# Optimization experiments

Hardware: AMD Instinct MI355X
Metric: run time of the kernel (lower is better)

## Reference

```python
import jax, jax.numpy as jnp
import numpy as np

NUM_HEADS = 8
CHUNK = 64
TOP_K = 5


def setup_inputs() -> dict:
    key = jax.random.key(0)
    ks = jax.random.split(key, 5)
    D = 512
    x = jax.random.normal(ks[0], (1, 2048, D), dtype=jnp.float32)
    s = 0.02
    Wq = jax.random.normal(ks[1], (D, D), dtype=jnp.float32) * s
    Wk = jax.random.normal(ks[2], (D, D), dtype=jnp.float32) * s
    Wv = jax.random.normal(ks[3], (D, D), dtype=jnp.float32) * s
    Wo = jax.random.normal(ks[4], (D, D), dtype=jnp.float32) * s
    return {"x": x, "Wq": Wq, "Wk": Wk, "Wv": Wv, "Wo": Wo}


def reference(x, Wq, Wk, Wv, Wo):
    B, S, D = x.shape
    H = NUM_HEADS
    hd = D // H
    scale = hd ** -0.5
    C = S // CHUNK  # number of chunks

    def split_heads(t):
        return t.reshape(B, S, H, hd).transpose(0, 2, 1, 3)  # [B,H,S,hd]

    Q = split_heads(x @ Wq)
    K = split_heads(x @ Wk)
    V = split_heads(x @ Wv)

    # chunked K/V: [B,H,C,chunk,hd]
    Kc = K.reshape(B, H, C, CHUNK, hd)
    Vc = V.reshape(B, H, C, CHUNK, hd)

    # chunk descriptors: mean-pooled keys per chunk -> [B,H,C,hd]
    chunk_keys = Kc.mean(axis=3)

    # route each query to top-k chunks by scaled similarity
    sims = jnp.einsum('bhsd,bhcd->bhsc', Q, chunk_keys) * scale  # [B,H,S,C]
    _, idx = jax.lax.top_k(sims, TOP_K)  # [B,H,S,K]

    # gather selected K/V chunk blocks: [B,H,S,K,chunk,hd]
    idx_flat = idx.reshape(B, H, S * TOP_K)[:, :, :, None, None]
    Kg = jnp.take_along_axis(Kc, idx_flat, axis=2).reshape(B, H, S, TOP_K, CHUNK, hd)
    Vg = jnp.take_along_axis(Vc, idx_flat, axis=2).reshape(B, H, S, TOP_K, CHUNK, hd)

    # sparse block attention over the K*chunk gathered keys per query
    scores = jnp.einsum('bhsd,bhskcd->bhskc', Q, Kg) * scale
    attn = jax.nn.softmax(scores.reshape(B, H, S, TOP_K * CHUNK), axis=-1)
    attn = attn.reshape(B, H, S, TOP_K, CHUNK)
    out = jnp.einsum('bhskc,bhskcd->bhsd', attn, Vg)  # [B,H,S,hd]

    out = out.transpose(0, 2, 1, 3).reshape(B, S, D)
    return out @ Wo
```

## Files before the change

### kernel.cpp

```cpp
#include <hip/hip_runtime.h>
#include <hip/hip_bf16.h>
#include <math.h>

#define S_LEN 2048
#define D_DIM 512
#define H_NUM 8
#define HD    64
#define C_NUM 32
#define TOPK  5
#define SCALE 0.125f
#define QCAP  1024
#define ATILES 16

typedef __attribute__((ext_vector_type(8))) short bf16x8;
typedef __attribute__((ext_vector_type(4))) float f32x4;
typedef __attribute__((ext_vector_type(4))) unsigned short us4;

__device__ __forceinline__ unsigned short f2b(float f) {
    __hip_bfloat16 h = __float2bfloat16(f);
    unsigned short u;
    __builtin_memcpy(&u, &h, 2);
    return u;
}
__device__ __forceinline__ bf16x8 pack8(float4 a, float4 b) {
    bf16x8 r;
    r[0] = (short)f2b(a.x); r[1] = (short)f2b(a.y);
    r[2] = (short)f2b(a.z); r[3] = (short)f2b(a.w);
    r[4] = (short)f2b(b.x); r[5] = (short)f2b(b.y);
    r[6] = (short)f2b(b.z); r[7] = (short)f2b(b.w);
    return r;
}
__device__ __forceinline__ float b2f(unsigned short u) {
    __hip_bfloat16 h;
    __builtin_memcpy(&h, &u, 2);
    return __bfloat162float(h);
}

#define BM 64
#define BN 64
#define BK 32

__device__ __forceinline__ void gemm_body(const float* __restrict__ A,
                                          const float* __restrict__ B,
                                          float* __restrict__ C,
                                          int M, int N, int K,
                                          int bx, int by) {
    __shared__ float As[BK][BM + 4];
    __shared__ float Bs[BK][BN];

    const int t  = threadIdx.x;
    const int tx = t & 15;
    const int ty = t >> 4;
    const int m0 = by * BM;
    const int n0 = bx * BN;

    float4 acc0 = make_float4(0.f,0.f,0.f,0.f);
    float4 acc1 = make_float4(0.f,0.f,0.f,0.f);
    float4 acc2 = make_float4(0.f,0.f,0.f,0.f);
    float4 acc3 = make_float4(0.f,0.f,0.f,0.f);

    const int ar = t >> 3;
    const int ac = (t & 7) * 4;
    const int br = t >> 4;
    const int bc = (t & 15) * 4;

    float4 a0, a1, b0, b1;
    auto LD = [&](int k0) {
        a0 = *(const float4*)&A[(size_t)(m0 + ar)      * K + k0 + ac];
        a1 = *(const float4*)&A[(size_t)(m0 + ar + 32) * K + k0 + ac];
        b0 = *(const float4*)&B[(size_t)(k0 + br)      * N + n0 + bc];
        b1 = *(const float4*)&B[(size_t)(k0 + br + 16) * N + n0 + bc];
    };

    LD(0);
    for (int k0 = 0; k0 < K; k0 += BK) {
        __syncthreads();
        As[ac+0][ar]    = a0.x; As[ac+1][ar]    = a0.y; As[ac+2][ar]    = a0.z; As[ac+3][ar]    = a0.w;
        As[ac+0][ar+32] = a1.x; As[ac+1][ar+32] = a1.y; As[ac+2][ar+32] = a1.z; As[ac+3][ar+32] = a1.w;
        *(float4*)&Bs[br][bc]      = b0;
        *(float4*)&Bs[br + 16][bc] = b1;
        __syncthreads();

        if (k0 + BK < K) LD(k0 + BK);

        #pragma unroll
        for (int kk = 0; kk < BK; ++kk) {
            float4 a = *(const float4*)&As[kk][ty * 4];
            float4 b = *(const float4*)&Bs[kk][tx * 4];
            acc0.x += a.x*b.x; acc0.y += a.x*b.y; acc0.z += a.x*b.z; acc0.w += a.x*b.w;
            acc1.x += a.y*b.x; acc1.y += a.y*b.y; acc1.z += a.y*b.z; acc1.w += a.y*b.w;
            acc2.x += a.z*b.x; acc2.y += a.z*b.y; acc2.z += a.z*b.z; acc2.w += a.z*b.w;
            acc3.x += a.w*b.x; acc3.y += a.w*b.y; acc3.z += a.w*b.z; acc3.w += a.w*b.w;
        }
    }

    *(float4*)&C[(size_t)(m0 + ty*4 + 0) * N + n0 + tx*4] = acc0;
    *(float4*)&C[(size_t)(m0 + ty*4 + 1) * N + n0 + tx*4] = acc1;
    *(float4*)&C[(size_t)(m0 + ty*4 + 2) * N + n0 + tx*4] = acc2;
    *(float4*)&C[(size_t)(m0 + ty*4 + 3) * N + n0 + tx*4] = acc3;
}

__global__ __launch_bounds__(256) void gemm_qkv(const float* __restrict__ A,
                                                const float* __restrict__ Wq,
                                                const float* __restrict__ Wk,
                                                float* __restrict__ Qb,
                                                float* __restrict__ Kb) {
    const float* B = (blockIdx.z == 0) ? Wq : Wk;
    float*       C = (blockIdx.z == 0) ? Qb : Kb;
    gemm_body(A, B, C, S_LEN, D_DIM, D_DIM, blockIdx.x, blockIdx.y);
}

template <bool ABF16, bool CBF16>
__device__ __forceinline__ void gemm_bf16_body(const void* __restrict__ Aptr,
                                               const float* __restrict__ B,
                                               void* __restrict__ Cptr,
                                               int M, int N, int K,
                                               int bx, int by) {
    __shared__ unsigned short As[64][72];
    __shared__ unsigned short Bs[64][72];

    const int t  = threadIdx.x;
    const int m0 = by * 64;
    const int n0 = bx * 64;
    const int rl = t >> 2;
    const int c4 = (t & 3) * 16;

    const int lane = t & 63, w = t >> 6, lr = lane & 15, quad = lane >> 4;

    f32x4 acc[4] = {{0.f,0.f,0.f,0.f},{0.f,0.f,0.f,0.f},
                    {0.f,0.f,0.f,0.f},{0.f,0.f,0.f,0.f}};

    float4 fa[4]; bf16x8 ba[2]; float4 fb[4];
    auto LDA = [&](int k0) {
        if (ABF16) {
            const unsigned short* A = (const unsigned short*)Aptr;
            ba[0] = *(const bf16x8*)&A[(size_t)(m0 + rl) * K + k0 + c4];
            ba[1] = *(const bf16x8*)&A[(size_t)(m0 + rl) * K + k0 + c4 + 8];
        } else {
            const float* A = (const float*)Aptr;
            const float* p = &A[(size_t)(m0 + rl) * K + k0 + c4];
            fa[0] = *(const float4*)&p[0];  fa[1] = *(const float4*)&p[4];
            fa[2] = *(const float4*)&p[8];  fa[3] = *(const float4*)&p[12];
        }
    };
    auto LDB = [&](int k0) {
        const float* p = &B[(size_t)(k0 + rl) * N + n0 + c4];
        fb[0] = *(const float4*)&p[0];  fb[1] = *(const float4*)&p[4];
        fb[2] = *(const float4*)&p[8];  fb[3] = *(const float4*)&p[12];
    };

    LDA(0); LDB(0);
    for (int k0 = 0; k0 < K; k0 += 64) {
        __syncthreads();
        if (ABF16) {
            *(bf16x8*)&As[rl][c4]     = ba[0];
            *(bf16x8*)&As[rl][c4 + 8] = ba[1];
        } else {
            *(bf16x8*)&As[rl][c4]     = pack8(fa[0], fa[1]);
            *(bf16x8*)&As[rl][c4 + 8] = pack8(fa[2], fa[3]);
        }
        #pragma unroll
        for (int f = 0; f < 4; ++f) {
            float4 v = fb[f];
            Bs[c4 + f*4 + 0][rl] = f2b(v.x);
            Bs[c4 + f*4 + 1][rl] = f2b(v.y);
            Bs[c4 + f*4 + 2][rl] = f2b(v.z);
            Bs[c4 + f*4 + 3][rl] = f2b(v.w);
        }
        __syncthreads();

        if (k0 + 64 < K) { LDA(k0 + 64); LDB(k0 + 64); }

        bf16x8 a0 = *(const bf16x8*)&As[w * 16 + lr][quad * 8];
        bf16x8 a1 = *(const bf16x8*)&As[w * 16 + lr][32 + quad * 8];
        #pragma unroll
        for (int nt = 0; nt < 4; ++nt) {
            bf16x8 b0 = *(const bf16x8*)&Bs[nt * 16 + lr][quad * 8];
            bf16x8 b1 = *(const bf16x8*)&Bs[nt * 16 + lr][32 + quad * 8];
            acc[nt] = __builtin_amdgcn_mfma_f32_16x16x32_bf16(a0, b0, acc[nt], 0, 0, 0);
            acc[nt] = __builtin_amdgcn_mfma_f32_16x16x32_bf16(a1, b1, acc[nt], 0, 0, 0);
        }
    }

    #pragma unroll
    for (int nt = 0; nt < 4; ++nt)
        #pragma unroll
        for (int r = 0; r < 4; ++r) {
            int m = m0 + w * 16 + quad * 4 + r;
            int n = n0 + nt * 16 + lr;
            if (CBF16) ((unsigned short*)Cptr)[(size_t)m * N + n] = f2b(acc[nt][r]);
            else       ((float*)Cptr)[(size_t)m * N + n] = acc[nt][r];
        }
}

__global__ __launch_bounds__(256) void gemm_v(const float* __restrict__ x,
                                              const float* __restrict__ Wv,
                                              unsigned short* __restrict__ Vbf,
                                              int* __restrict__ cur) {
    if (blockIdx.x == 0 && blockIdx.y == 0) cur[threadIdx.x] = 0;
    gemm_bf16_body<false, true>(x, Wv, Vbf, S_LEN, D_DIM, D_DIM,
                                blockIdx.x, blockIdx.y);
}

__global__ __launch_bounds__(256) void gemm_out(const unsigned short* __restrict__ Obn,
                                                const float* __restrict__ Wo,
                                                float* __restrict__ out) {
    gemm_bf16_body<true, false>(Obn, Wo, out, S_LEN, D_DIM, D_DIM,
                                blockIdx.x, blockIdx.y);
}

__global__ __launch_bounds__(256) void chunk_keys_kernel(const float* __restrict__ K,
                                                         float* __restrict__ ck) {
    int i = blockIdx.x * 256 + threadIdx.x;
    int c = i >> 9;
    int d = i & 511;
    const float* p = K + (size_t)c * 64 * D_DIM + d;
    float sum = 0.f;
    #pragma unroll
    for (int r = 0; r < 64; ++r) sum += p[(size_t)r * D_DIM];
    ck[(size_t)c * D_DIM + d] = sum * (1.0f / 64.0f);
}

__global__ __launch_bounds__(256) void sims_topk(const float* __restrict__ Q,
                                                 const float* __restrict__ ck,
                                                 int* __restrict__ cur,
                                                 unsigned short* __restrict__ qlist) {
    __shared__ float qtile[64][68];
    __shared__ float cks[32][68];
    __shared__ float simsb[64][36];
    __shared__ int   lds_cnt[32];
    __shared__ int   lds_base[32];

    const int t  = threadIdx.x;
    const int s0 = blockIdx.x * 64;
    const int h  = blockIdx.y;

    if (t < 32) lds_cnt[t] = 0;

    {
        int r = t >> 2;
        #pragma unroll
        for (int i = 0; i < 4; ++i) {
            int cf4 = (t & 3) * 4 + i;
            *(float4*)&qtile[r][cf4 * 4] =
                *(const float4*)&Q[(size_t)(s0 + r) * D_DIM + h * HD + cf4 * 4];
        }
    }
    for (int i = t; i < C_NUM * 16; i += 256) {
        int c = i >> 4, df4 = i & 15;
        *(float4*)&cks[c][df4 * 4] =
            *(const float4*)&ck[(size_t)c * D_DIM + h * HD + df4 * 4];
    }
    __syncthreads();

    {
        const int sl = t >> 2, g = t & 3;
        float sa[8] = {0.f,0.f,0.f,0.f,0.f,0.f,0.f,0.f};
        #pragma unroll
        for (int d4 = 0; d4 < 16; ++d4) {
            float4 q4 = *(const float4*)&qtile[sl][d4 * 4];
            #pragma unroll
            for (int j = 0; j < 8; ++j) {
                float4 c4 = *(const float4*)&cks[g * 8 + j][d4 * 4];
                sa[j] += q4.x*c4.x + q4.y*c4.y + q4.z*c4.z + q4.w*c4.w;
            }
        }
        *(float4*)&simsb[sl][g*8 + 0] = make_float4(sa[0], sa[1], sa[2], sa[3]);
        *(float4*)&simsb[sl][g*8 + 4] = make_float4(sa[4], sa[5], sa[6], sa[7]);
    }
    __syncthreads();

    int csel[TOPK], lpos[TOPK];
    if (t < 64) {
        float sv[32];
        #pragma unroll
        for (int cq = 0; cq < 8; ++cq) {
            float4 v = *(const float4*)&simsb[t][cq * 4];
            sv[cq*4+0] = v.x; sv[cq*4+1] = v.y; sv[cq*4+2] = v.z; sv[cq*4+3] = v.w;
        }
        #pragma unroll
        for (int k = 0; k < TOPK; ++k) {
            float best = -INFINITY; int bi = 0;
            #pragma unroll
            for (int cc = 0; cc < 32; ++cc) {
                bool gt = sv[cc] > best;
                best = gt ? sv[cc] : best;
                bi   = gt ? cc : bi;
            }
            #pragma unroll
            for (int cc = 0; cc < 32; ++cc)
                if (cc == bi) sv[cc] = -INFINITY;
            csel[k] = bi;
            lpos[k] = atomicAdd(&lds_cnt[bi], 1);
        }
    }
    __syncthreads();

    if (t < 32) lds_base[t] = atomicAdd(&cur[h * 32 + t], lds_cnt[t]);
    __syncthreads();

    if (t < 64) {
        #pragma unroll
        for (int k = 0; k < TOPK; ++k) {
            int c = csel[k];
            int pos = lds_base[c] + lpos[k];
            if (pos < QCAP)
                qlist[(size_t)(h * 32 + c) * QCAP + pos] =
                    (unsigned short)((s0 + t) | (k << 11));
        }
    }
}

__global__ __launch_bounds__(256) void moc_attn6(const float* __restrict__ Q,
                                                 const float* __restrict__ K,
                                                 const unsigned short* __restrict__ Vbf,
                                                 const int* __restrict__ cnt,
                                                 const unsigned short* __restrict__ qlist,
                                                 float* __restrict__ lpart,
                                                 float* __restrict__ Opart) {
    __shared__ unsigned short Qs[64][72];
    __shared__ unsigned short Ks[64][72];
    __shared__ unsigned short VT[64][72];
    __shared__ unsigned short Ps[64][72];
    __shared__ unsigned short slist[64];

    const int hc = blockIdx.y;
    const int h  = hc >> 5;
    const int c  = hc & 31;
    const int g  = blockIdx.x;
    const int t  = threadIdx.x;

    const int count = min(cnt[hc], QCAP);
    const int base  = g * 64;
    if (base >= count) return;
    const int lim = min(count - base, 64);

    const float* Kb = K + ((size_t)c * 64) * D_DIM + h * HD;
    const unsigned short* Vb = Vbf + ((size_t)c * 64) * D_DIM + h * HD;
    const unsigned short* list = qlist + (size_t)hc * QCAP + base;

    {
        const int j  = t >> 2;
        const int d0 = (t & 3) * 16;

        const float* kr = Kb + (size_t)j * D_DIM + d0;
        float4 k0 = *(const float4*)&kr[0],  k1 = *(const float4*)&kr[4];
        float4 k2 = *(const float4*)&kr[8],  k3 = *(const float4*)&kr[12];
        *(bf16x8*)&Ks[j][d0]     = pack8(k0, k1);
        *(bf16x8*)&Ks[j][d0 + 8] = pack8(k2, k3);

        const unsigned short* vr = Vb + (size_t)j * D_DIM + d0;
        bf16x8 v0 = *(const bf16x8*)&vr[0];
        bf16x8 v1 = *(const bf16x8*)&vr[8];
        #pragma unroll
        for (int i = 0; i < 8; ++i) {
            VT[d0 + i][j]     = (unsigned short)v0[i];
            VT[d0 + 8 + i][j] = (unsigned short)v1[i];
        }

        unsigned short pv = (j < lim) ? list[j] : (unsigned short)0xFFFF;
        if ((t & 3) == 0) slist[j] = pv;
        int s = (pv == 0xFFFF) ? 0 : (int)(pv & 2047);
        const float* qr = Q + (size_t)s * D_DIM + h * HD + d0;
        float4 q0 = *(const float4*)&qr[0],  q1 = *(const float4*)&qr[4];
        float4 q2 = *(const float4*)&qr[8],  q3 = *(const float4*)&qr[12];
        *(bf16x8*)&Qs[j][d0]     = pack8(q0, q1);
        *(bf16x8*)&Qs[j][d0 + 8] = pack8(q2, q3);
    }
    __syncthreads();

    const int lane = t & 63;
    const int w    = t >> 6;
    const int lr   = lane & 15;
    const int quad = lane >> 4;

    bf16x8 aq0 = *(const bf16x8*)&Qs[w * 16 + lr][quad * 8];
    bf16x8 aq1 = *(const bf16x8*)&Qs[w * 16 + lr][32 + quad * 8];

    f32x4 acc[4];
    #pragma unroll
    for (int kt = 0; kt < 4; ++kt) {
        bf16x8 b0 = *(const bf16x8*)&Ks[kt * 16 + lr][quad * 8];
        bf16x8 b1 = *(const bf16x8*)&Ks[kt * 16 + lr][32 + quad * 8];
        f32x4 z = {0.f, 0.f, 0.f, 0.f};
        z = __builtin_amdgcn_mfma_f32_16x16x32_bf16(aq0, b0, z, 0, 0, 0);
        z = __builtin_amdgcn_mfma_f32_16x16x32_bf16(aq1, b1, z, 0, 0, 0);
        acc[kt] = z;
    }

    unsigned short pb[4][4];
    float dsum[4] = {0.f, 0.f, 0.f, 0.f};
    #pragma unroll
    for (int kt = 0; kt < 4; ++kt) {
        #pragma unroll
        for (int r = 0; r < 4; ++r) {
            unsigned short u = f2b(__expf(acc[kt][r] * SCALE));
            pb[kt][r] = u;
            dsum[r] += b2f(u);
        }
    }
    #pragma unroll
    for (int r = 0; r < 4; ++r) {
        float v = dsum[r];
        v += __shfl_xor(v, 1, 64);
        v += __shfl_xor(v, 2, 64);
        v += __shfl_xor(v, 4, 64);
        v += __shfl_xor(v, 8, 64);
        dsum[r] = v;
    }
    if (lr == 0) {
        #pragma unroll
        for (int r = 0; r < 4; ++r) {
            unsigned short sv = slist[w * 16 + quad * 4 + r];
            if (sv != 0xFFFF) {
                int kk = sv >> 11, s = sv & 2047;
                lpart[((size_t)kk * H_NUM + h) * S_LEN + s] = dsum[r];
            }
        }
    }

    #pragma unroll
    for (int kt = 0; kt < 4; ++kt)
        #pragma unroll
        for (int r = 0; r < 4; ++r)
            Ps[w * 16 + quad * 4 + r][kt * 16 + lr] = pb[kt][r];

    bf16x8 ap0 = *(const bf16x8*)&Ps[w * 16 + lr][quad * 8];
    bf16x8 ap1 = *(const bf16x8*)&Ps[w * 16 + lr][32 + quad * 8];

    #pragma unroll
    for (int dt = 0; dt < 4; ++dt) {
        bf16x8 b0 = *(const bf16x8*)&VT[dt * 16 + lr][quad * 8];
        bf16x8 b1 = *(const bf16x8*)&VT[dt * 16 + lr][32 + quad * 8];
        f32x4 z = {0.f, 0.f, 0.f, 0.f};
        z = __builtin_amdgcn_mfma_f32_16x16x32_bf16(ap0, b0, z, 0, 0, 0);
        z = __builtin_amdgcn_mfma_f32_16x16x32_bf16(ap1, b1, z, 0, 0, 0);
        #pragma unroll
        for (int r = 0; r < 4; ++r) {
            unsigned short sv = slist[w * 16 + quad * 4 + r];
            if (sv != 0xFFFF) {
                int kk = sv >> 11, s = sv & 2047;
                Opart[((((size_t)kk * H_NUM + h) * S_LEN + s) * HD) + dt * 16 + lr] = z[r];
            }
        }
    }
}

__global__ __launch_bounds__(256) void reduce_norm(const float4* __restrict__ Opart4,
                                                   const float* __restrict__ lpart,
                                                   unsigned short* __restrict__ Obn) {
    int i = blockIdx.x * 256 + threadIdx.x;
    int s    = i >> 7;
    int col4 = i & 127;
    int h    = col4 >> 4;
    int f4   = col4 & 15;
    float4 acc = make_float4(0.f,0.f,0.f,0.f);
    float  den = 0.f;
    #pragma unroll
    for (int k = 0; k < TOPK; ++k) {
        size_t slot = ((size_t)k * H_NUM + h) * S_LEN + s;
        float4 v = Opart4[slot * 16 + f4];
        acc.x += v.x; acc.y += v.y; acc.z += v.z; acc.w += v.w;
        den += lpart[slot];
    }
    float inv = 1.0f / den;
    us4 o;
    o[0] = f2b(acc.x * inv); o[1] = f2b(acc.y * inv);
    o[2] = f2b(acc.z * inv); o[3] = f2b(acc.w * inv);
    *(us4*)&Obn[(size_t)i * 4] = o;
}

extern "C" void kernel_launch(void* const* d_in, const int* in_sizes, int n_in,
                              void* d_out, int out_size, void* d_ws, size_t ws_size,
                              hipStream_t stream) {
    const float* x  = (const float*)d_in[0];
    const float* Wq = (const float*)d_in[1];
    const float* Wk = (const float*)d_in[2];
    const float* Wv = (const float*)d_in[3];
    const float* Wo = (const float*)d_in[4];
    float* out = (float*)d_out;

    const size_t SD = (size_t)S_LEN * D_DIM;
    float* ws    = (float*)d_ws;
    float* Qb    = ws;
    float* Kb    = Qb + SD;
    unsigned short* Vbf = (unsigned short*)(Kb + SD);
    float* ck    = (float*)(Vbf + SD);
    float* lpart = ck + (size_t)C_NUM * D_DIM;
    int*   curb  = (int*)(lpart + (size_t)TOPK * H_NUM * S_LEN);
    unsigned short* qlst = (unsigned short*)(curb + 256);
    float* Opart = (float*)(qlst + (size_t)256 * QCAP);
    unsigned short* Obn = (unsigned short*)Qb;

    dim3 qkgrid(D_DIM / BN, S_LEN / BM, 2);
    gemm_qkv<<<qkgrid, 256, 0, stream>>>(x, Wq, Wk, Qb, Kb);

    dim3 vgrid(D_DIM / 64, S_LEN / 64);
    gemm_v<<<vgrid, 256, 0, stream>>>(x, Wv, Vbf, curb);

    chunk_keys_kernel<<<(C_NUM * D_DIM) / 256, 256, 0, stream>>>(Kb, ck);

    dim3 rgrid(S_LEN / 64, H_NUM);
    sims_topk<<<rgrid, 256, 0, stream>>>(Qb, ck, curb, qlst);

    dim3 agrid(ATILES, H_NUM * C_NUM);
    moc_attn6<<<agrid, 256, 0, stream>>>(Qb, Kb, Vbf, curb, qlst, lpart, Opart);

    reduce_norm<<<(int)(SD / 4 / 256), 256, 0, stream>>>((const float4*)Opart, lpart, Obn);

    dim3 ogrid(D_DIM / 64, S_LEN / 64);
    gemm_out<<<ogrid, 256, 0, stream>>>(Obn, Wo, out);
}
```

Before: 159.4 us.

## Merge QKV projections into one launch and fuse partial reduction into output GEMM

```diff
diff --git a/kernel.cpp b/kernel.cpp
--- a/kernel.cpp
+++ b/kernel.cpp
@@ -14,7 +14,6 @@
 
 typedef __attribute__((ext_vector_type(8))) short bf16x8;
 typedef __attribute__((ext_vector_type(4))) float f32x4;
-typedef __attribute__((ext_vector_type(4))) unsigned short us4;
 
 __device__ __forceinline__ unsigned short f2b(float f) {
     __hip_bfloat16 h = __float2bfloat16(f);
@@ -100,24 +99,13 @@
     *(float4*)&C[(size_t)(m0 + ty*4 + 3) * N + n0 + tx*4] = acc3;
 }
 
-__global__ __launch_bounds__(256) void gemm_qkv(const float* __restrict__ A,
-                                                const float* __restrict__ Wq,
-                                                const float* __restrict__ Wk,
-                                                float* __restrict__ Qb,
-                                                float* __restrict__ Kb) {
-    const float* B = (blockIdx.z == 0) ? Wq : Wk;
-    float*       C = (blockIdx.z == 0) ? Qb : Kb;
-    gemm_body(A, B, C, S_LEN, D_DIM, D_DIM, blockIdx.x, blockIdx.y);
-}
-
-template <bool ABF16, bool CBF16>
-__device__ __forceinline__ void gemm_bf16_body(const void* __restrict__ Aptr,
-                                               const float* __restrict__ B,
-                                               void* __restrict__ Cptr,
-                                               int M, int N, int K,
-                                               int bx, int by) {
-    __shared__ unsigned short As[64][72];
-    __shared__ unsigned short Bs[64][72];
+__device__ __forceinline__ void gemm_v_body(const float* __restrict__ A,
+                                            const float* __restrict__ B,
+                                            unsigned short* __restrict__ C,
+                                            int M, int N, int K,
+                                            int bx, int by) {
+    __shared__ unsigned short Asv[64][72];
+    __shared__ unsigned short Bsv[64][72];
 
     const int t  = threadIdx.x;
     const int m0 = by * 64;
@@ -130,18 +118,11 @@
     f32x4 acc[4] = {{0.f,0.f,0.f,0.f},{0.f,0.f,0.f,0.f},
                     {0.f,0.f,0.f,0.f},{0.f,0.f,0.f,0.f}};
 
-    float4 fa[4]; bf16x8 ba[2]; float4 fb[4];
+    float4 fa[4], fb[4];
     auto LDA = [&](int k0) {
-        if (ABF16) {
-            const unsigned short* A = (const unsigned short*)Aptr;
-            ba[0] = *(const bf16x8*)&A[(size_t)(m0 + rl) * K + k0 + c4];
-            ba[1] = *(const bf16x8*)&A[(size_t)(m0 + rl) * K + k0 + c4 + 8];
-        } else {
-            const float* A = (const float*)Aptr;
-            const float* p = &A[(size_t)(m0 + rl) * K + k0 + c4];
-            fa[0] = *(const float4*)&p[0];  fa[1] = *(const float4*)&p[4];
-            fa[2] = *(const float4*)&p[8];  fa[3] = *(const float4*)&p[12];
-        }
+        const float* p = &A[(size_t)(m0 + rl) * K + k0 + c4];
+        fa[0] = *(const float4*)&p[0];  fa[1] = *(const float4*)&p[4];
+        fa[2] = *(const float4*)&p[8];  fa[3] = *(const float4*)&p[12];
     };
     auto LDB = [&](int k0) {
         const float* p = &B[(size_t)(k0 + rl) * N + n0 + c4];
@@ -152,31 +133,26 @@
     LDA(0); LDB(0);
     for (int k0 = 0; k0 < K; k0 += 64) {
         __syncthreads();
-        if (ABF16) {
-            *(bf16x8*)&As[rl][c4]     = ba[0];
-            *(bf16x8*)&As[rl][c4 + 8] = ba[1];
-        } else {
-            *(bf16x8*)&As[rl][c4]     = pack8(fa[0], fa[1]);
-            *(bf16x8*)&As[rl][c4 + 8] = pack8(fa[2], fa[3]);
-        }
+        *(bf16x8*)&Asv[rl][c4]     = pack8(fa[0], fa[1]);
+        *(bf16x8*)&Asv[rl][c4 + 8] = pack8(fa[2], fa[3]);
         #pragma unroll
         for (int f = 0; f < 4; ++f) {
             float4 v = fb[f];
-            Bs[c4 + f*4 + 0][rl] = f2b(v.x);
-            Bs[c4 + f*4 + 1][rl] = f2b(v.y);
-            Bs[c4 + f*4 + 2][rl] = f2b(v.z);
-            Bs[c4 + f*4 + 3][rl] = f2b(v.w);
+            Bsv[c4 + f*4 + 0][rl] = f2b(v.x);
+            Bsv[c4 + f*4 + 1][rl] = f2b(v.y);
+            Bsv[c4 + f*4 + 2][rl] = f2b(v.z);
+            Bsv[c4 + f*4 + 3][rl] = f2b(v.w);
         }
         __syncthreads();
 
         if (k0 + 64 < K) { LDA(k0 + 64); LDB(k0 + 64); }
 
-        bf16x8 a0 = *(const bf16x8*)&As[w * 16 + lr][quad * 8];
-        bf16x8 a1 = *(const bf16x8*)&As[w * 16 + lr][32 + quad * 8];
+        bf16x8 a0 = *(const bf16x8*)&Asv[w * 16 + lr][quad * 8];
+        bf16x8 a1 = *(const bf16x8*)&Asv[w * 16 + lr][32 + quad * 8];
         #pragma unroll
         for (int nt = 0; nt < 4; ++nt) {
-            bf16x8 b0 = *(const bf16x8*)&Bs[nt * 16 + lr][quad * 8];
-            bf16x8 b1 = *(const bf16x8*)&Bs[nt * 16 + lr][32 + quad * 8];
+            bf16x8 b0 = *(const bf16x8*)&Bsv[nt * 16 + lr][quad * 8];
+            bf16x8 b1 = *(const bf16x8*)&Bsv[nt * 16 + lr][32 + quad * 8];
             acc[nt] = __builtin_amdgcn_mfma_f32_16x16x32_bf16(a0, b0, acc[nt], 0, 0, 0);
             acc[nt] = __builtin_amdgcn_mfma_f32_16x16x32_bf16(a1, b1, acc[nt], 0, 0, 0);
         }
@@ -188,25 +164,26 @@
         for (int r = 0; r < 4; ++r) {
             int m = m0 + w * 16 + quad * 4 + r;
             int n = n0 + nt * 16 + lr;
-            if (CBF16) ((unsigned short*)Cptr)[(size_t)m * N + n] = f2b(acc[nt][r]);
-            else       ((float*)Cptr)[(size_t)m * N + n] = acc[nt][r];
-        }
-}
-
-__global__ __launch_bounds__(256) void gemm_v(const float* __restrict__ x,
-                                              const float* __restrict__ Wv,
-                                              unsigned short* __restrict__ Vbf,
-                                              int* __restrict__ cur) {
-    if (blockIdx.x == 0 && blockIdx.y == 0) cur[threadIdx.x] = 0;
-    gemm_bf16_body<false, true>(x, Wv, Vbf, S_LEN, D_DIM, D_DIM,
-                                blockIdx.x, blockIdx.y);
-}
-
-__global__ __launch_bounds__(256) void gemm_out(const unsigned short* __restrict__ Obn,
-                                                const float* __restrict__ Wo,
-                                                float* __restrict__ out) {
-    gemm_bf16_body<true, false>(Obn, Wo, out, S_LEN, D_DIM, D_DIM,
-                                blockIdx.x, blockIdx.y);
+            C[(size_t)m * N + n] = f2b(acc[nt][r]);
+        }
+}
+
+__global__ __launch_bounds__(256) void gemm_qkvz(const float* __restrict__ x,
+                                                 const float* __restrict__ Wq,
+                                                 const float* __restrict__ Wk,
+                                                 const float* __restrict__ Wv,
+                                                 float* __restrict__ Qb,
+                                                 float* __restrict__ Kb,
+                                                 unsigned short* __restrict__ Vbf,
+                                                 int* __restrict__ cur) {
+    if (blockIdx.z == 2) {
+        if (blockIdx.x == 0 && blockIdx.y == 0) cur[threadIdx.x] = 0;
+        gemm_v_body(x, Wv, Vbf, S_LEN, D_DIM, D_DIM, blockIdx.x, blockIdx.y);
+    } else {
+        const float* B = (blockIdx.z == 0) ? Wq : Wk;
+        float*       C = (blockIdx.z == 0) ? Qb : Kb;
+        gemm_body(x, B, C, S_LEN, D_DIM, D_DIM, blockIdx.x, blockIdx.y);
+    }
 }
 
 __global__ __launch_bounds__(256) void chunk_keys_kernel(const float* __restrict__ K,
@@ -446,28 +423,96 @@
     }
 }
 
-__global__ __launch_bounds__(256) void reduce_norm(const float4* __restrict__ Opart4,
-                                                   const float* __restrict__ lpart,
-                                                   unsigned short* __restrict__ Obn) {
-    int i = blockIdx.x * 256 + threadIdx.x;
-    int s    = i >> 7;
-    int col4 = i & 127;
-    int h    = col4 >> 4;
-    int f4   = col4 & 15;
-    float4 acc = make_float4(0.f,0.f,0.f,0.f);
-    float  den = 0.f;
-    #pragma unroll
-    for (int k = 0; k < TOPK; ++k) {
-        size_t slot = ((size_t)k * H_NUM + h) * S_LEN + s;
-        float4 v = Opart4[slot * 16 + f4];
-        acc.x += v.x; acc.y += v.y; acc.z += v.z; acc.w += v.w;
-        den += lpart[slot];
-    }
-    float inv = 1.0f / den;
-    us4 o;
-    o[0] = f2b(acc.x * inv); o[1] = f2b(acc.y * inv);
-    o[2] = f2b(acc.z * inv); o[3] = f2b(acc.w * inv);
-    *(us4*)&Obn[(size_t)i * 4] = o;
+__global__ __launch_bounds__(256) void gemm_out_fused(const float* __restrict__ Opart,
+                                                      const float* __restrict__ lpart,
+                                                      const float* __restrict__ Wo,
+                                                      float* __restrict__ out) {
+    __shared__ unsigned short As[64][72];
+    __shared__ unsigned short Bs[64][72];
+
+    const int t  = threadIdx.x;
+    const int m0 = blockIdx.y * 64;
+    const int n0 = blockIdx.x * 64;
+    const int rl = t >> 2;
+    const int c4 = (t & 3) * 16;
+
+    const int lane = t & 63, w = t >> 6, lr = lane & 15, quad = lane >> 4;
+    const int N = D_DIM, K = D_DIM;
+
+    f32x4 acc[4] = {{0.f,0.f,0.f,0.f},{0.f,0.f,0.f,0.f},
+                    {0.f,0.f,0.f,0.f},{0.f,0.f,0.f,0.f}};
+
+    float4 fa[4], fb[4];
+    auto LDA = [&](int k0) {
+        const int kcol = k0 + c4;
+        const int h  = kcol >> 6;
+        const int d0 = kcol & 63;
+        const int m  = m0 + rl;
+        fa[0] = make_float4(0.f,0.f,0.f,0.f);
+        fa[1] = make_float4(0.f,0.f,0.f,0.f);
+        fa[2] = make_float4(0.f,0.f,0.f,0.f);
+        fa[3] = make_float4(0.f,0.f,0.f,0.f);
+        float den = 0.f;
+        #pragma unroll
+        for (int r = 0; r < TOPK; ++r) {
+            size_t slot = ((size_t)r * H_NUM + h) * S_LEN + m;
+            const float* P = Opart + slot * HD + d0;
+            float4 v0 = *(const float4*)&P[0],  v1 = *(const float4*)&P[4];
+            float4 v2 = *(const float4*)&P[8],  v3 = *(const float4*)&P[12];
+            fa[0].x += v0.x; fa[0].y += v0.y; fa[0].z += v0.z; fa[0].w += v0.w;
+            fa[1].x += v1.x; fa[1].y += v1.y; fa[1].z += v1.z; fa[1].w += v1.w;
+            fa[2].x += v2.x; fa[2].y += v2.y; fa[2].z += v2.z; fa[2].w += v2.w;
+            fa[3].x += v3.x; fa[3].y += v3.y; fa[3].z += v3.z; fa[3].w += v3.w;
+            den += lpart[slot];
+        }
+        float inv = 1.0f / den;
+        #pragma unroll
+        for (int f = 0; f < 4; ++f) {
+            fa[f].x *= inv; fa[f].y *= inv; fa[f].z *= inv; fa[f].w *= inv;
+        }
+    };
+    auto LDB = [&](int k0) {
+        const float* p = &Wo[(size_t)(k0 + rl) * N + n0 + c4];
+        fb[0] = *(const float4*)&p[0];  fb[1] = *(const float4*)&p[4];
+        fb[2] = *(const float4*)&p[8];  fb[3] = *(const float4*)&p[12];
+    };
+
+    LDA(0); LDB(0);
+    for (int k0 = 0; k0 < K; k0 += 64) {
+        __syncthreads();
+        *(bf16x8*)&As[rl][c4]     = pack8(fa[0], fa[1]);
+        *(bf16x8*)&As[rl][c4 + 8] = pack8(fa[2], fa[3]);
+        #pragma unroll
+        for (int f = 0; f < 4; ++f) {
+            float4 v = fb[f];
+            Bs[c4 + f*4 + 0][rl] = f2b(v.x);
+            Bs[c4 + f*4 + 1][rl] = f2b(v.y);
+            Bs[c4 + f*4 + 2][rl] = f2b(v.z);
+            Bs[c4 + f*4 + 3][rl] = f2b(v.w);
+        }
+        __syncthreads();
+
+        if (k0 + 64 < K) { LDA(k0 + 64); LDB(k0 + 64); }
+
+        bf16x8 a0 = *(const bf16x8*)&As[w * 16 + lr][quad * 8];
+        bf16x8 a1 = *(const bf16x8*)&As[w * 16 + lr][32 + quad * 8];
+        #pragma unroll
+        for (int nt = 0; nt < 4; ++nt) {
+            bf16x8 b0 = *(const bf16x8*)&Bs[nt * 16 + lr][quad * 8];
+            bf16x8 b1 = *(const bf16x8*)&Bs[nt * 16 + lr][32 + quad * 8];
+            acc[nt] = __builtin_amdgcn_mfma_f32_16x16x32_bf16(a0, b0, acc[nt], 0, 0, 0);
+            acc[nt] = __builtin_amdgcn_mfma_f32_16x16x32_bf16(a1, b1, acc[nt], 0, 0, 0);
+        }
+    }
+
+    #pragma unroll
+    for (int nt = 0; nt < 4; ++nt)
+        #pragma unroll
+        for (int r = 0; r < 4; ++r) {
+            int m = m0 + w * 16 + quad * 4 + r;
+            int n = n0 + nt * 16 + lr;
+            out[(size_t)m * N + n] = acc[nt][r];
+        }
 }
 
 extern "C" void kernel_launch(void* const* d_in, const int* in_sizes, int n_in,
@@ -490,13 +535,9 @@
     int*   curb  = (int*)(lpart + (size_t)TOPK * H_NUM * S_LEN);
     unsigned short* qlst = (unsigned short*)(curb + 256);
     float* Opart = (float*)(qlst + (size_t)256 * QCAP);
-    unsigned short* Obn = (unsigned short*)Qb;
-
-    dim3 qkgrid(D_DIM / BN, S_LEN / BM, 2);
-    gemm_qkv<<<qkgrid, 256, 0, stream>>>(x, Wq, Wk, Qb, Kb);
-
-    dim3 vgrid(D_DIM / 64, S_LEN / 64);
-    gemm_v<<<vgrid, 256, 0, stream>>>(x, Wv, Vbf, curb);
+
+    dim3 pgrid(D_DIM / 64, S_LEN / 64, 3);
+    gemm_qkvz<<<pgrid, 256, 0, stream>>>(x, Wq, Wk, Wv, Qb, Kb, Vbf, curb);
 
     chunk_keys_kernel<<<(C_NUM * D_DIM) / 256, 256, 0, stream>>>(Kb, ck);
 
@@ -506,8 +547,6 @@
     dim3 agrid(ATILES, H_NUM * C_NUM);
     moc_attn6<<<agrid, 256, 0, stream>>>(Qb, Kb, Vbf, curb, qlst, lpart, Opart);
 
-    reduce_norm<<<(int)(SD / 4 / 256), 256, 0, stream>>>((const float4*)Opart, lpart, Obn);
-
     dim3 ogrid(D_DIM / 64, S_LEN / 64);
-    gemm_out<<<ogrid, 256, 0, stream>>>(Obn, Wo, out);
-}
+    gemm_out_fused<<<ogrid, 256, 0, stream>>>(Opart, lpart, Wo, out);
+}
```

New measurement: 171.2 us. 1.07x slower.
